# Kernel optimization log

Hardware: AMD Instinct MI355X
Metric: run time of the kernel (lower is better)

Reference implementation:

```python
import jax, jax.numpy as jnp
import numpy as np

N_NODES = 100000
N_EDGES = 1600000
N_GRAPHS = 2048
D = 128
H = 128
EPS = 1e-5


def gcn_conv(x, src, dst, W, b, n):
    # x: [N, Din], W: [Din, Dout]; GCN with added self-loops and symmetric norm
    xw = x @ W                                       # [N, Dout]
    deg = jnp.zeros((n,), x.dtype).at[dst].add(1.0) + 1.0  # deg of A+I (counted on dst)
    dinv = jax.lax.rsqrt(deg)                        # [N]
    norm = dinv[src] * dinv[dst]                     # [E]
    msg = xw[src] * norm[:, None]                    # [E, Dout] gather + scale
    agg = jax.ops.segment_sum(msg, dst, num_segments=n)
    agg = agg + xw * (dinv * dinv)[:, None]          # self-loop contribution
    return agg + b


def gru_step_h0(x, W_ih, W_hh, b_ih, b_hh):
    # single GRU step with h0 = 0 (PyTorch gate order r, z, n)
    h0 = jnp.zeros_like(x)
    gi = x @ W_ih.T + b_ih                           # [G, 3H]
    gh = h0 @ W_hh.T + b_hh                          # [G, 3H] (zeros + b_hh)
    ir, iz, inn = jnp.split(gi, 3, axis=-1)
    hr, hz, hn = jnp.split(gh, 3, axis=-1)
    r = jax.nn.sigmoid(ir + hr)
    z = jax.nn.sigmoid(iz + hz)
    n = jnp.tanh(inn + r * hn)
    return (1.0 - z) * n + z * h0


def setup_inputs() -> dict:
    key = jax.random.key(0)
    ks = jax.random.split(key, 10)
    x = jax.random.normal(ks[0], (N_NODES, D), jnp.float32)
    edge_index = jax.random.randint(ks[1], (2, N_EDGES), 0, N_NODES, jnp.int32)
    batch = jnp.sort(jax.random.randint(ks[2], (N_NODES,), 0, N_GRAPHS, jnp.int32))
    s = 1.0 / np.sqrt(H)
    return {
        "x": x,
        "edge_index": edge_index,
        "batch": batch,
        "W1": jax.random.normal(ks[3], (D, H), jnp.float32) * s,
        "b1": jnp.zeros((H,), jnp.float32),
        "W2": jax.random.normal(ks[4], (H, H), jnp.float32) * s,
        "b2": jnp.zeros((H,), jnp.float32),
        "W_ih": jax.random.normal(ks[5], (3 * H, H), jnp.float32) * s,
        "W_hh": jax.random.normal(ks[6], (3 * H, H), jnp.float32) * s,
        "b_ih": jnp.zeros((3 * H,), jnp.float32),
        "b_hh": jnp.zeros((3 * H,), jnp.float32),
        "W_lin": jax.random.normal(ks[7], (1, H), jnp.float32) * s,
        "b_lin": jnp.zeros((1,), jnp.float32),
    }


def reference(x, edge_index, batch, W1, b1, W2, b2, W_ih, W_hh, b_ih, b_hh, W_lin, b_lin):
    src, dst = edge_index[0], edge_index[1]
    n = x.shape[0]
    h = jax.nn.relu(gcn_conv(x, src, dst, W1, b1, n))
    h = gcn_conv(h, src, dst, W2, b2, n)
    # global_mean_pool over graph ids
    sums = jax.ops.segment_sum(h, batch, num_segments=N_GRAPHS)
    cnts = jax.ops.segment_sum(jnp.ones((n,), h.dtype), batch, num_segments=N_GRAPHS)
    g = sums / jnp.maximum(cnts, 1.0)[:, None]       # [G, H]
    # dropout p=0.5 in eval mode -> identity
    g = gru_step_h0(g, W_ih, W_hh, b_ih, b_hh)
    g = jax.nn.relu(g)
    mu = jnp.mean(g, axis=-1, keepdims=True)
    var = jnp.mean(jnp.square(g - mu), axis=-1, keepdims=True)
    g = (g - mu) * jax.lax.rsqrt(var + EPS)          # layer_norm, no affine
    return g @ W_lin.T + b_lin                       # [G, 1]
```

## Files before the change

kernel.cpp:

```cpp
#include <hip/hip_runtime.h>
#include <hip/hip_bf16.h>
#include <math.h>

#define DHID 128
#define SH 7
#define BIN_T 2048
#define CAPSH 12
#define SRC_SH 13

typedef __attribute__((ext_vector_type(8))) short bf16x8;
typedef __attribute__((ext_vector_type(4))) float f32x4;
typedef __attribute__((ext_vector_type(2))) float f32x2;

__device__ __forceinline__ int atomAddI(int* p, int v) {
    return __hip_atomic_fetch_add(p, v, __ATOMIC_RELAXED, __HIP_MEMORY_SCOPE_AGENT);
}
__device__ __forceinline__ float bf_lo(unsigned u) { return __uint_as_float(u << 16); }
__device__ __forceinline__ float bf_hi(unsigned u) { return __uint_as_float(u & 0xffff0000u); }
__device__ __forceinline__ f32x2 bfpk(unsigned u) {
    f32x2 r;
    r.x = __uint_as_float(u << 16);
    r.y = __uint_as_float(u & 0xffff0000u);
    return r;
}
__device__ __forceinline__ unsigned short bf16_1(float f) {
    unsigned u = __float_as_uint(f);
    u += 0x7fffu + ((u >> 16) & 1u);
    return (unsigned short)(u >> 16);
}
__device__ __forceinline__ unsigned pack_bf16x2(float a, float b) {
    unsigned ua = __float_as_uint(a);
    unsigned ub = __float_as_uint(b);
    ua = (ua + 0x7fffu + ((ua >> 16) & 1u)) >> 16;
    ub = (ub + 0x7fffu + ((ub >> 16) & 1u)) & 0xffff0000u;
    return ua | ub;
}

__global__ __launch_bounds__(256) void bin_edges(const int* __restrict__ src,
                                                 const int* __restrict__ dst,
                                                 int* __restrict__ bcur,
                                                 unsigned* __restrict__ staged,
                                                 const float* __restrict__ W1,
                                                 const float* __restrict__ W2,
                                                 const float* __restrict__ Wih,
                                                 unsigned short* __restrict__ Wt1,
                                                 unsigned short* __restrict__ Wt2,
                                                 unsigned short* __restrict__ Wihb,
                                                 int E, int NB, int nb_bin) {
    int t = threadIdx.x;
    if (blockIdx.x >= nb_bin) {
        int idx = (blockIdx.x - nb_bin) * 256 + t;
        if (idx < 16384) {
            int k = idx >> 7, n = idx & 127;
            Wt1[n * 128 + k] = bf16_1(W1[idx]);
        } else if (idx < 32768) {
            int j = idx - 16384;
            int k = j >> 7, n = j & 127;
            Wt2[n * 128 + k] = bf16_1(W2[j]);
        } else if (idx < 32768 + 49152) {
            int j = idx - 32768;
            Wihb[j] = bf16_1(Wih[j]);
        }
        return;
    }
    __shared__ int lh[1024], lbase[1024], lcur[1024];
    int e0 = blockIdx.x * BIN_T;
    int eend = min(e0 + BIN_T, E);
    for (int i = t; i < NB; i += 256) { lh[i] = 0; lcur[i] = 0; }
    __syncthreads();
    int sv[8], dv[8];
#pragma unroll
    for (int i = 0; i < 8; i++) {
        int e = e0 + t + i * 256;
        if (e < eend) { sv[i] = src[e]; dv[i] = dst[e]; }
        else { sv[i] = 0; dv[i] = -1; }
    }
#pragma unroll
    for (int i = 0; i < 8; i++)
        if (dv[i] >= 0) atomicAdd(&lh[dv[i] >> SH], 1);
    __syncthreads();
    for (int i = t; i < NB; i += 256)
        lbase[i] = lh[i] ? atomAddI(&bcur[i], lh[i]) : 0;
    __syncthreads();
#pragma unroll
    for (int i = 0; i < 8; i++) {
        if (dv[i] >= 0) {
            int d = dv[i];
            int b = d >> SH;
            int pos = lbase[b] + atomicAdd(&lcur[b], 1);
            staged[((size_t)b << CAPSH) + pos] =
                (unsigned)sv[i] | ((unsigned)(d & ((1 << SH) - 1)) << 24);
        }
    }
}

__global__ __launch_bounds__(256) void scatter_gemm(const unsigned* __restrict__ staged,
                                                    const int* __restrict__ bcur,
                                                    int* __restrict__ off,
                                                    float* __restrict__ dinv,
                                                    int* __restrict__ rec,
                                                    int N, int E, int NB,
                                                    const float* __restrict__ Xf,
                                                    const unsigned short* __restrict__ Wt,
                                                    unsigned short* __restrict__ Y) {
    __shared__ __align__(16) unsigned char smem[52224];
    const int tid = threadIdx.x;
    if (blockIdx.x < NB) {
        int* hist = (int*)smem;
        int* sh   = (int*)(smem + 8192);
        int t = tid;
        int b = blockIdx.x;
        int node0 = b << SH;

        int s0 = (t < b) ? bcur[t] : 0;
        int s1 = (256 + t < b) ? bcur[256 + t] : 0;
        int s2 = (512 + t < b) ? bcur[512 + t] : 0;
        int s3 = (768 + t < b) ? bcur[768 + t] : 0;
        int s = s0 + s1 + s2 + s3;
#pragma unroll
        for (int o = 1; o < 64; o <<= 1) s += __shfl_xor(s, o);
        if ((t & 63) == 0) sh[t >> 6] = s;
        __syncthreads();
        int base = sh[0] + sh[1] + sh[2] + sh[3];
        __syncthreads();

        for (int i = t; i < 2048; i += 256) hist[i] = 0;
        __syncthreads();
        int cnt_b = bcur[b];
        const unsigned* st = staged + ((size_t)b << CAPSH);
        for (int j = t; j < cnt_b; j += 256) {
            unsigned w = st[j];
            int key = (int)((w >> 24) << 4) | (int)((w & 0xFFFFFFu) >> SRC_SH);
            atomicAdd(&hist[key], 1);
        }
        __syncthreads();

        int loc[16];
        int run = 0;
        if (t < 128) {
            int base16 = t * 16;
#pragma unroll
            for (int i = 0; i < 16; i++) { loc[i] = run; run += hist[base16 + i]; }
        }
        sh[t] = (t < 128) ? run : 0;
        __syncthreads();
#pragma unroll
        for (int o = 1; o < 256; o <<= 1) {
            int x = (t >= o) ? sh[t - o] : 0;
            __syncthreads();
            sh[t] += x;
            __syncthreads();
        }
        int excl = sh[t] - run;
        if (t < 128) {
            int base16 = t * 16;
#pragma unroll
            for (int i = 0; i < 16; i++) hist[base16 + i] = base + excl + loc[i];
            int node = node0 + t;
            if (node < N) {
                off[node] = base + excl;
                dinv[node] = rsqrtf((float)run + 1.0f);
            }
        }
        if (b == NB - 1 && t == 0) off[N] = E;
        __syncthreads();

        for (int j = t; j < cnt_b; j += 256) {
            unsigned w = st[j];
            int key = (int)((w >> 24) << 4) | (int)((w & 0xFFFFFFu) >> SRC_SH);
            int pos = atomicAdd(&hist[key], 1);
            rec[pos] = (int)(w & 0xFFFFFFu);
        }
    } else {
        unsigned short* Xs = (unsigned short*)smem;
        unsigned short* Ws = (unsigned short*)(smem + 17408);
        {
            const uint4* W4 = (const uint4*)Wt;
#pragma unroll
            for (int i = 0; i < 8; i++) {
                int idx = tid + i * 256;
                int r = idx >> 4, c8 = idx & 15;
                *(uint4*)&Ws[r * 136 + c8 * 8] = W4[idx];
            }
        }
        const int row0 = (blockIdx.x - NB) * 64;
        {
            const float4* X4 = (const float4*)Xf;
#pragma unroll
            for (int i = 0; i < 8; i++) {
                int idx = tid + i * 256;
                int r = idx >> 5, c4 = idx & 31;
                float4 v = make_float4(0.f, 0.f, 0.f, 0.f);
                if (row0 + r < N) v = X4[(size_t)(row0 + r) * 32 + c4];
                uint2 pk = make_uint2(pack_bf16x2(v.x, v.y), pack_bf16x2(v.z, v.w));
                *(uint2*)&Xs[r * 136 + c4 * 4] = pk;
            }
        }
        __syncthreads();

        const int lane = tid & 63;
        const int wv = tid >> 6;
        const int m = lane & 15, quad = lane >> 4;
        const int wrow = wv * 16;

        f32x4 acc[8];
#pragma unroll
        for (int i = 0; i < 8; i++) acc[i] = (f32x4){0.f, 0.f, 0.f, 0.f};

#pragma unroll
        for (int kc = 0; kc < 4; kc++) {
            bf16x8 a = *(const bf16x8*)&Xs[(wrow + m) * 136 + kc * 32 + quad * 8];
#pragma unroll
            for (int nt = 0; nt < 8; nt++) {
                bf16x8 bfr = *(const bf16x8*)&Ws[(nt * 16 + m) * 136 + kc * 32 + quad * 8];
                acc[nt] = __builtin_amdgcn_mfma_f32_16x16x32_bf16(a, bfr, acc[nt], 0, 0, 0);
            }
        }

#pragma unroll
        for (int r = 0; r < 4; r++) {
            int lrow = wrow + quad * 4 + r;
#pragma unroll
            for (int nt = 0; nt < 8; nt++)
                Xs[lrow * 136 + nt * 16 + m] = bf16_1(acc[nt][r]);
        }
        __syncthreads();
#pragma unroll
        for (int i = 0; i < 4; i++) {
            int idx = tid + i * 256;
            int r = idx >> 4, c8 = idx & 15;
            if (row0 + r < N)
                *(uint4*)&Y[(size_t)(row0 + r) * DHID + c8 * 8] =
                    *(const uint4*)&Xs[r * 136 + c8 * 8];
        }
    }
}

__global__ __launch_bounds__(256) void aggregate(const unsigned short* __restrict__ A,
                                                 const float* __restrict__ dinv,
                                                 const int* __restrict__ off,
                                                 const int* __restrict__ rec,
                                                 const float* __restrict__ bias,
                                                 unsigned short* __restrict__ Bout,
                                                 int N, int mode) {
    int node = blockIdx.x * 4 + (threadIdx.x >> 6);
    if (node >= N) return;
    int lane = threadIdx.x & 63;
    int q  = lane >> 4;
    int ql = lane & 15;
    float di = dinv[node];
    f32x2 acc[4];
    if (q == 0) {
        f32x2 s2 = {di * di, di * di};
        uint4 v = ((const uint4*)(A + (size_t)node * DHID))[ql];
        const float4* bb = (const float4*)(bias + ql * 8);
        float4 b0 = bb[0], b1 = bb[1];
        acc[0] = bfpk(v.x) * s2 + (f32x2){b0.x, b0.y};
        acc[1] = bfpk(v.y) * s2 + (f32x2){b0.z, b0.w};
        acc[2] = bfpk(v.z) * s2 + (f32x2){b1.x, b1.y};
        acc[3] = bfpk(v.w) * s2 + (f32x2){b1.z, b1.w};
    } else {
#pragma unroll
        for (int i = 0; i < 4; i++) acc[i] = (f32x2){0.f, 0.f};
    }
    int j = off[node] + q;
    int jend = off[node + 1];
    if (j + 4 < jend) {
        int s0 = rec[j], s1 = rec[j + 4];
        for (; j + 12 < jend; j += 8) {
            int n0 = rec[j + 8], n1 = rec[j + 12];
            uint4 v0 = ((const uint4*)(A + (size_t)s0 * DHID))[ql];
            uint4 v1 = ((const uint4*)(A + (size_t)s1 * DHID))[ql];
            float w0s = dinv[s0] * di;
            float w1s = dinv[s1] * di;
            f32x2 w0 = {w0s, w0s};
            f32x2 w1 = {w1s, w1s};
            acc[0] += bfpk(v0.x) * w0;  acc[0] += bfpk(v1.x) * w1;
            acc[1] += bfpk(v0.y) * w0;  acc[1] += bfpk(v1.y) * w1;
            acc[2] += bfpk(v0.z) * w0;  acc[2] += bfpk(v1.z) * w1;
            acc[3] += bfpk(v0.w) * w0;  acc[3] += bfpk(v1.w) * w1;
            s0 = n0; s1 = n1;
        }
        {
            uint4 v0 = ((const uint4*)(A + (size_t)s0 * DHID))[ql];
            uint4 v1 = ((const uint4*)(A + (size_t)s1 * DHID))[ql];
            float w0s = dinv[s0] * di;
            float w1s = dinv[s1] * di;
            f32x2 w0 = {w0s, w0s};
            f32x2 w1 = {w1s, w1s};
            acc[0] += bfpk(v0.x) * w0;  acc[0] += bfpk(v1.x) * w1;
            acc[1] += bfpk(v0.y) * w0;  acc[1] += bfpk(v1.y) * w1;
            acc[2] += bfpk(v0.z) * w0;  acc[2] += bfpk(v1.z) * w1;
            acc[3] += bfpk(v0.w) * w0;  acc[3] += bfpk(v1.w) * w1;
            j += 8;
        }
    }
    if (j < jend) {
        int s0 = rec[j];
        uint4 v0 = ((const uint4*)(A + (size_t)s0 * DHID))[ql];
        float w0s = dinv[s0] * di;
        f32x2 w0 = {w0s, w0s};
        acc[0] += bfpk(v0.x) * w0;
        acc[1] += bfpk(v0.y) * w0;
        acc[2] += bfpk(v0.z) * w0;
        acc[3] += bfpk(v0.w) * w0;
    }
#pragma unroll
    for (int i = 0; i < 4; i++) {
        acc[i].x += __shfl_xor(acc[i].x, 16);
        acc[i].y += __shfl_xor(acc[i].y, 16);
        acc[i].x += __shfl_xor(acc[i].x, 32);
        acc[i].y += __shfl_xor(acc[i].y, 32);
    }
    if (q == 0) {
        if (mode == 1) {
#pragma unroll
            for (int i = 0; i < 4; i++) {
                acc[i].x = fmaxf(acc[i].x, 0.f);
                acc[i].y = fmaxf(acc[i].y, 0.f);
            }
        }
        uint4 pk;
        pk.x = pack_bf16x2(acc[0].x, acc[0].y);
        pk.y = pack_bf16x2(acc[1].x, acc[1].y);
        pk.z = pack_bf16x2(acc[2].x, acc[2].y);
        pk.w = pack_bf16x2(acc[3].x, acc[3].y);
        ((uint4*)(Bout + (size_t)node * DHID))[ql] = pk;
    }
}

__global__ __launch_bounds__(256) void tail_head(const unsigned short* __restrict__ B,
                                                 const int* __restrict__ batch,
                                                 const unsigned short* __restrict__ Wt2,
                                                 const float* __restrict__ b2,
                                                 const unsigned short* __restrict__ Wihb,
                                                 const float* __restrict__ b_ih,
                                                 const float* __restrict__ b_hh,
                                                 const float* __restrict__ W_lin,
                                                 const float* __restrict__ b_lin,
                                                 float* __restrict__ out,
                                                 int N, int G) {
    __shared__ float grow[128];
    __shared__ float psum[4][128];
    __shared__ float g2[128];
    __shared__ float gi[384];
    __shared__ float red[4];
    __shared__ int se[2];
    const int t = threadIdx.x;
    const int g = blockIdx.x;
    if (t < 2) {
        int target = g + t, lo = 0, hi = N;
        while (lo < hi) {
            int mid = (lo + hi) >> 1;
            if (batch[mid] < target) lo = mid + 1; else hi = mid;
        }
        se[t] = lo;
    }
    __syncthreads();
    const int s = se[0], e = se[1];

    const int c2 = t & 63;
    const int rh = t >> 6;
    float sx = 0.f, sy = 0.f;
    for (int r = s + rh; r < e; r += 4) {
        unsigned u = *(const unsigned*)(B + (size_t)r * DHID + c2 * 2);
        sx += bf_lo(u);
        sy += bf_hi(u);
    }
    *(float2*)&psum[rh][c2 * 2] = make_float2(sx, sy);
    __syncthreads();
    if (t < 128) {
        grow[t] = (psum[0][t] + psum[1][t] + psum[2][t] + psum[3][t]) /
                  fmaxf((float)(e - s), 1.0f);
    }
    __syncthreads();

    if (t < 128) {
        float a = 0.f;
        const uint4* wr = (const uint4*)(Wt2 + (size_t)t * DHID);
#pragma unroll
        for (int k8 = 0; k8 < 16; k8++) {
            uint4 wv = wr[k8];
            const float* gk = &grow[k8 * 8];
            a += bf_lo(wv.x) * gk[0] + bf_hi(wv.x) * gk[1]
               + bf_lo(wv.y) * gk[2] + bf_hi(wv.y) * gk[3]
               + bf_lo(wv.z) * gk[4] + bf_hi(wv.z) * gk[5]
               + bf_lo(wv.w) * gk[6] + bf_hi(wv.w) * gk[7];
        }
        g2[t] = a + b2[t];
    }
    __syncthreads();

    {
        float a0 = 0.f;
        const uint4* wr = (const uint4*)(Wihb + (size_t)t * DHID);
#pragma unroll
        for (int k8 = 0; k8 < 16; k8++) {
            uint4 wv = wr[k8];
            const float* gk = &g2[k8 * 8];
            a0 += bf_lo(wv.x) * gk[0] + bf_hi(wv.x) * gk[1]
                + bf_lo(wv.y) * gk[2] + bf_hi(wv.y) * gk[3]
                + bf_lo(wv.z) * gk[4] + bf_hi(wv.z) * gk[5]
                + bf_lo(wv.w) * gk[6] + bf_hi(wv.w) * gk[7];
        }
        gi[t] = a0;
    }
    if (t < 128) {
        float a1 = 0.f;
        const uint4* wr = (const uint4*)(Wihb + (size_t)(256 + t) * DHID);
#pragma unroll
        for (int k8 = 0; k8 < 16; k8++) {
            uint4 wv = wr[k8];
            const float* gk = &g2[k8 * 8];
            a1 += bf_lo(wv.x) * gk[0] + bf_hi(wv.x) * gk[1]
                + bf_lo(wv.y) * gk[2] + bf_hi(wv.y) * gk[3]
                + bf_lo(wv.z) * gk[4] + bf_hi(wv.z) * gk[5]
                + bf_lo(wv.w) * gk[6] + bf_hi(wv.w) * gk[7];
        }
        gi[256 + t] = a1;
    }
    __syncthreads();

    float y = 0.f, wl = 0.f;
    if (t < 128) {
        float d0 = gi[t], d1 = gi[128 + t], d2 = gi[256 + t];
        float rg = 1.f / (1.f + expf(-(d0 + b_ih[t] + b_hh[t])));
        float zg = 1.f / (1.f + expf(-(d1 + b_ih[128 + t] + b_hh[128 + t])));
        float ng = tanhf(d2 + b_ih[256 + t] + rg * b_hh[256 + t]);
        y = fmaxf((1.f - zg) * ng, 0.f);
        wl = W_lin[t];
    }
    auto blockSum = [&](float v) -> float {
#pragma unroll
        for (int o = 1; o < 64; o <<= 1) v += __shfl_xor(v, o);
        __syncthreads();
        if ((t & 63) == 0) red[t >> 6] = v;
        __syncthreads();
        return red[0] + red[1] + red[2] + red[3];
    };
    float mu = blockSum(y) * (1.f / 128.f);
    float dy = (t < 128) ? (y - mu) : 0.f;
    float var = blockSum(dy * dy) * (1.f / 128.f);
    float yn = dy * rsqrtf(var + 1e-5f);
    float tot = blockSum(yn * wl);
    if (t == 0) out[g] = tot + b_lin[0];
}

extern "C" void kernel_launch(void* const* d_in, const int* in_sizes, int n_in,
                              void* d_out, int out_size, void* d_ws, size_t ws_size,
                              hipStream_t stream) {
    const float* x     = (const float*)d_in[0];
    const int*   ei    = (const int*)d_in[1];
    const int*   batch = (const int*)d_in[2];
    const float* W1    = (const float*)d_in[3];
    const float* b1    = (const float*)d_in[4];
    const float* W2    = (const float*)d_in[5];
    const float* b2    = (const float*)d_in[6];
    const float* W_ih  = (const float*)d_in[7];
    const float* b_ih  = (const float*)d_in[9];
    const float* b_hh  = (const float*)d_in[10];
    const float* W_lin = (const float*)d_in[11];
    const float* b_lin = (const float*)d_in[12];
    float* out = (float*)d_out;

    const int N = in_sizes[0] / DHID;
    const int E = in_sizes[1] / 2;
    const int G = out_size;
    const int* src = ei;
    const int* dst = ei + E;
    const int NB = (N + (1 << SH) - 1) >> SH;

    auto align256 = [](size_t v) { return (v + 255) & ~(size_t)255; };
    char* p = (char*)d_ws;
    size_t used = 0;
    auto carve = [&](size_t bytes) -> char* {
        char* q = p + used;
        used += align256(bytes);
        return q;
    };

    int*   off    = (int*)carve(((size_t)N + 1) * 4);
    int*   bcur   = (int*)carve(1024 * 4);
    float* zbias  = (float*)carve(128 * 4);
    float* dinv   = (float*)carve((size_t)N * 4);
    unsigned* staged = (unsigned*)carve(((size_t)NB << CAPSH) * 4);
    int*   rec    = (int*)carve((size_t)E * 4);
    unsigned short* Wt1  = (unsigned short*)carve((size_t)128 * 128 * 2);
    unsigned short* Wt2  = (unsigned short*)carve((size_t)128 * 128 * 2);
    unsigned short* Wihb = (unsigned short*)carve((size_t)3 * 128 * 128 * 2);
    unsigned short* A    = (unsigned short*)carve((size_t)N * DHID * 2);
    unsigned short* B1b  = (unsigned short*)carve((size_t)N * DHID * 2);
    size_t matB = (size_t)N * DHID * 2;
    unsigned short* B2b;
    if (ws_size >= used + matB) {
        B2b = (unsigned short*)carve(matB);
    } else {
        B2b = (unsigned short*)d_in[0];
    }

    dim3 blk(256);
    int nb_g  = (N + 63) / 64;
    int nb_ag = (N + 3) / 4;
    int nb_bin = (E + BIN_T - 1) / BIN_T;
    int nb_wp  = (81920 + 255) / 256;

    hipMemsetAsync(bcur, 0, 1024 * 4 + 256 + 128 * 4, stream);
    bin_edges<<<nb_bin + nb_wp, blk, 0, stream>>>(src, dst, bcur, staged,
                                                  W1, W2, W_ih, Wt1, Wt2, Wihb,
                                                  E, NB, nb_bin);
    scatter_gemm<<<NB + nb_g, blk, 0, stream>>>(staged, bcur, off, dinv, rec,
                                                N, E, NB, x, Wt1, A);

    aggregate<<<nb_ag, blk, 0, stream>>>(A, dinv, off, rec, b1, B1b, N, 1);

    aggregate<<<nb_ag, blk, 0, stream>>>(B1b, dinv, off, rec, zbias, B2b, N, 0);

    tail_head<<<G, blk, 0, stream>>>(B2b, batch, Wt2, b2, Wihb, b_ih, b_hh,
                                     W_lin, b_lin, out, N, G);
}
```

Measured before the change: 333.8 us.

## Widen node bins and stage edge scatter through LDS for coalesced writes

Doubles the nodes per bin (fewer bins) and quadruples edges per binning block. Binned edges are first sorted locally in shared memory and then written contiguously to the staged buffer. The CSR build also sorts records in LDS before writing rec, so scattered global writes become coalesced ones. The cost is more shared memory per block (lower occupancy), an extra block-wide prefix scan, and a binary search per edge. The change also relies on per-bin capacity and memset sizes staying consistent with the new constants.

```diff
diff --git a/kernel.cpp b/kernel.cpp
--- a/kernel.cpp
+++ b/kernel.cpp
@@ -3,9 +3,9 @@
 #include <math.h>
 
 #define DHID 128
-#define SH 7
-#define BIN_T 2048
-#define CAPSH 12
+#define SH 8
+#define BIN_T 8192
+#define CAPSH 13
 #define SRC_SH 13
 
 typedef __attribute__((ext_vector_type(8))) short bf16x8;
@@ -63,34 +63,51 @@
         }
         return;
     }
-    __shared__ int lh[1024], lbase[1024], lcur[1024];
+    __shared__ int lh[512], lbase[512], lstart[512], lcur[512];
+    __shared__ int sh[256];
+    __shared__ unsigned sortbuf[8192];
     int e0 = blockIdx.x * BIN_T;
     int eend = min(e0 + BIN_T, E);
-    for (int i = t; i < NB; i += 256) { lh[i] = 0; lcur[i] = 0; }
-    __syncthreads();
-    int sv[8], dv[8];
-#pragma unroll
-    for (int i = 0; i < 8; i++) {
-        int e = e0 + t + i * 256;
-        if (e < eend) { sv[i] = src[e]; dv[i] = dst[e]; }
-        else { sv[i] = 0; dv[i] = -1; }
-    }
-#pragma unroll
-    for (int i = 0; i < 8; i++)
-        if (dv[i] >= 0) atomicAdd(&lh[dv[i] >> SH], 1);
-    __syncthreads();
-    for (int i = t; i < NB; i += 256)
-        lbase[i] = lh[i] ? atomAddI(&bcur[i], lh[i]) : 0;
-    __syncthreads();
-#pragma unroll
-    for (int i = 0; i < 8; i++) {
-        if (dv[i] >= 0) {
-            int d = dv[i];
-            int b = d >> SH;
-            int pos = lbase[b] + atomicAdd(&lcur[b], 1);
-            staged[((size_t)b << CAPSH) + pos] =
-                (unsigned)sv[i] | ((unsigned)(d & ((1 << SH) - 1)) << 24);
-        }
+    int cnt_blk = eend - e0;
+    for (int i = t; i < 512; i += 256) { lh[i] = 0; lcur[i] = 0; }
+    __syncthreads();
+    for (int e = e0 + t; e < eend; e += 256)
+        atomicAdd(&lh[dst[e] >> SH], 1);
+    __syncthreads();
+    {
+        int a0 = lh[2 * t], a1 = lh[2 * t + 1];
+        lbase[2 * t]     = a0 ? atomAddI(&bcur[2 * t], a0) : 0;
+        lbase[2 * t + 1] = a1 ? atomAddI(&bcur[2 * t + 1], a1) : 0;
+        int run = a0 + a1;
+        sh[t] = run;
+        __syncthreads();
+#pragma unroll
+        for (int o = 1; o < 256; o <<= 1) {
+            int x = (t >= o) ? sh[t - o] : 0;
+            __syncthreads();
+            sh[t] += x;
+            __syncthreads();
+        }
+        int excl = sh[t] - run;
+        lstart[2 * t] = excl;
+        lstart[2 * t + 1] = excl + a0;
+    }
+    __syncthreads();
+    for (int e = e0 + t; e < eend; e += 256) {
+        int d = dst[e];
+        int b = d >> SH;
+        int slot = lstart[b] + atomicAdd(&lcur[b], 1);
+        sortbuf[slot] = (unsigned)src[e] | ((unsigned)(d & ((1 << SH) - 1)) << 24);
+    }
+    __syncthreads();
+    for (int i = t; i < cnt_blk; i += 256) {
+        unsigned w = sortbuf[i];
+        int lo = 0, hi = 511;
+        while (lo < hi) {
+            int mid = (lo + hi + 1) >> 1;
+            if (lstart[mid] <= i) lo = mid; else hi = mid - 1;
+        }
+        staged[((size_t)lo << CAPSH) + lbase[lo] + (i - lstart[lo])] = w;
     }
 }
 
@@ -107,16 +124,15 @@
     const int tid = threadIdx.x;
     if (blockIdx.x < NB) {
         int* hist = (int*)smem;
-        int* sh   = (int*)(smem + 8192);
+        int* sh   = (int*)(smem + 16384);
+        unsigned* sbuf = (unsigned*)(smem + 17408);
         int t = tid;
         int b = blockIdx.x;
         int node0 = b << SH;
 
         int s0 = (t < b) ? bcur[t] : 0;
         int s1 = (256 + t < b) ? bcur[256 + t] : 0;
-        int s2 = (512 + t < b) ? bcur[512 + t] : 0;
-        int s3 = (768 + t < b) ? bcur[768 + t] : 0;
-        int s = s0 + s1 + s2 + s3;
+        int s = s0 + s1;
 #pragma unroll
         for (int o = 1; o < 64; o <<= 1) s += __shfl_xor(s, o);
         if ((t & 63) == 0) sh[t >> 6] = s;
@@ -124,7 +140,7 @@
         int base = sh[0] + sh[1] + sh[2] + sh[3];
         __syncthreads();
 
-        for (int i = t; i < 2048; i += 256) hist[i] = 0;
+        for (int i = t; i < 4096; i += 256) hist[i] = 0;
         __syncthreads();
         int cnt_b = bcur[b];
         const unsigned* st = staged + ((size_t)b << CAPSH);
@@ -137,12 +153,10 @@
 
         int loc[16];
         int run = 0;
-        if (t < 128) {
-            int base16 = t * 16;
-#pragma unroll
-            for (int i = 0; i < 16; i++) { loc[i] = run; run += hist[base16 + i]; }
-        }
-        sh[t] = (t < 128) ? run : 0;
+        int base16 = t * 16;
+#pragma unroll
+        for (int i = 0; i < 16; i++) { loc[i] = run; run += hist[base16 + i]; }
+        sh[t] = run;
         __syncthreads();
 #pragma unroll
         for (int o = 1; o < 256; o <<= 1) {
@@ -152,15 +166,13 @@
             __syncthreads();
         }
         int excl = sh[t] - run;
-        if (t < 128) {
-            int base16 = t * 16;
-#pragma unroll
-            for (int i = 0; i < 16; i++) hist[base16 + i] = base + excl + loc[i];
-            int node = node0 + t;
-            if (node < N) {
-                off[node] = base + excl;
-                dinv[node] = rsqrtf((float)run + 1.0f);
-            }
+#pragma unroll
+        for (int i = 0; i < 16; i++) hist[base16 + i] = excl + loc[i];
+
+        int node = node0 + t;
+        if (node < N) {
+            off[node] = base + excl;
+            dinv[node] = rsqrtf((float)run + 1.0f);
         }
         if (b == NB - 1 && t == 0) off[N] = E;
         __syncthreads();
@@ -168,9 +180,12 @@
         for (int j = t; j < cnt_b; j += 256) {
             unsigned w = st[j];
             int key = (int)((w >> 24) << 4) | (int)((w & 0xFFFFFFu) >> SRC_SH);
-            int pos = atomicAdd(&hist[key], 1);
-            rec[pos] = (int)(w & 0xFFFFFFu);
-        }
+            int slot = atomicAdd(&hist[key], 1);
+            sbuf[slot] = w & 0xFFFFFFu;
+        }
+        __syncthreads();
+        for (int i = t; i < cnt_b; i += 256)
+            rec[base + i] = (int)sbuf[i];
     } else {
         unsigned short* Xs = (unsigned short*)smem;
         unsigned short* Ws = (unsigned short*)(smem + 17408);
@@ -480,7 +495,7 @@
     };
 
     int*   off    = (int*)carve(((size_t)N + 1) * 4);
-    int*   bcur   = (int*)carve(1024 * 4);
+    int*   bcur   = (int*)carve(512 * 4);
     float* zbias  = (float*)carve(128 * 4);
     float* dinv   = (float*)carve((size_t)N * 4);
     unsigned* staged = (unsigned*)carve(((size_t)NB << CAPSH) * 4);
@@ -504,7 +519,7 @@
     int nb_bin = (E + BIN_T - 1) / BIN_T;
     int nb_wp  = (81920 + 255) / 256;
 
-    hipMemsetAsync(bcur, 0, 1024 * 4 + 256 + 128 * 4, stream);
+    hipMemsetAsync(bcur, 0, 512 * 4 + 128 * 4, stream);
     bin_edges<<<nb_bin + nb_wp, blk, 0, stream>>>(src, dst, bcur, staged,
                                                   W1, W2, W_ih, Wt1, Wt2, Wihb,
                                                   E, NB, nb_bin);
```

New measurement: 349.1 us. 4.6% more time.
